# Optimization experiments

Hardware: AMD Instinct MI355X
Metric: run time of the kernel (lower is better)

Reference implementation:

```python
import jax, jax.numpy as jnp
import numpy as np

B, T, D, U = 64, 1024, 300, 300


def setup_inputs() -> dict:
    key = jax.random.key(0)
    ks = jax.random.split(key, 12)
    inputs = jax.random.normal(ks[0], (B, T, D), jnp.float32)
    lengths = jax.random.randint(ks[1], (B,), T // 2, T + 1)
    mask = jnp.arange(T)[None, :] < lengths[:, None]  # [B,T] bool

    def w(k, shape, fan_in):
        return jax.random.normal(k, shape, jnp.float32) * (1.0 / np.sqrt(fan_in))

    # Keras GRU (reset_after=True): kernel [D,3U], recurrent_kernel [U,3U], bias [2,3U]
    k_fwd = w(ks[2], (D, 3 * U), D)
    rk_fwd = w(ks[3], (U, 3 * U), U)
    b_fwd = jnp.zeros((2, 3 * U), jnp.float32)
    k_bwd = w(ks[4], (D, 3 * U), D)
    rk_bwd = w(ks[5], (U, 3 * U), U)
    b_bwd = jnp.zeros((2, 3 * U), jnp.float32)
    w_fc = w(ks[6], (2 * U, U), 2 * U)
    b_fc = jnp.zeros((U,), jnp.float32)
    return {
        "inputs": inputs, "mask": mask,
        "k_fwd": k_fwd, "rk_fwd": rk_fwd, "b_fwd": b_fwd,
        "k_bwd": k_bwd, "rk_bwd": rk_bwd, "b_bwd": b_bwd,
        "w_fc": w_fc, "b_fc": b_fc, "training": 0,
    }


def _gru_dir(x, mask, kernel, rkernel, bias):
    """Keras GRU v2 (reset_after=True), zero_output_for_mask, state frozen on masked steps.
    x: [B,T,D], mask: [B,T] bool -> (ys [B,T,U], h_final [B,U])"""
    b_in, b_rec = bias[0], bias[1]
    u = rkernel.shape[0]
    # precompute input projections for all timesteps (cuDNN-style hoisting)
    xp = jnp.einsum('btd,dk->btk', x, kernel) + b_in  # [B,T,3U]

    def step(h, inp):
        xt, mt = inp  # xt: [B,3U], mt: [B]
        rp = h @ rkernel + b_rec  # [B,3U]
        xz, xr, xh = jnp.split(xt, 3, axis=-1)
        rz, rr, rh = jnp.split(rp, 3, axis=-1)
        z = jax.nn.sigmoid(xz + rz)
        r = jax.nn.sigmoid(xr + rr)
        hh = jnp.tanh(xh + r * rh)
        h_new = z * h + (1.0 - z) * hh
        m = mt[:, None]
        h_carry = jnp.where(m, h_new, h)       # state does not update on masked steps
        y = jnp.where(m, h_new, jnp.zeros_like(h_new))  # zero_output_for_mask
        return h_carry, y

    h0 = jnp.zeros((x.shape[0], u), x.dtype)
    h_final, ys = jax.lax.scan(step, h0, (xp.transpose(1, 0, 2), mask.T))
    return ys.transpose(1, 0, 2), h_final


def reference(inputs, mask, k_fwd, rk_fwd, b_fwd, k_bwd, rk_bwd, b_bwd, w_fc, b_fc, training):
    mask = mask.astype(bool)
    x = inputs  # Dropout is identity at inference (training=0)
    y_f, h_f = _gru_dir(x, mask, k_fwd, rk_fwd, b_fwd)
    # backward direction: process reversed sequence/mask, then re-reverse outputs
    y_b, h_b = _gru_dir(x[:, ::-1], mask[:, ::-1], k_bwd, rk_bwd, b_bwd)
    y_b = y_b[:, ::-1]
    output = jnp.concatenate([y_f, y_b], axis=-1)  # [B,T,2U]
    state = jax.nn.relu(jnp.concatenate([h_f, h_b], axis=-1) @ w_fc + b_fc)  # [B,U]
    return output, state
```

## Files before the change

kernel.cpp:

```cpp
#include <hip/hip_runtime.h>
#include <hip/hip_bf16.h>


#define B_   64
#define T_   1024
#define D_   300
#define U_   300
#define NU   900
#define KP   320
#define NP   960
#define XPW  912
#define KB_  10
#define KRES 2
#define HSP  328
#define FRAGS_PER_DIR 570
#define NRESF 114
#define NWGM 4

typedef short short8 __attribute__((ext_vector_type(8)));
typedef float floatx4 __attribute__((ext_vector_type(4)));

__device__ __forceinline__ float b2f_bits(unsigned short u) {
  union { unsigned int i; float f; } v; v.i = ((unsigned int)u) << 16; return v.f;
}
__device__ __forceinline__ unsigned short f2b(float f) {
  __hip_bfloat16 h = __float2bfloat16(f);
  return *reinterpret_cast<unsigned short*>(&h);
}

__global__ __launch_bounds__(64) void k_detect(const unsigned int* __restrict__ xw,
                                               const unsigned char* __restrict__ mb,
                                               int* __restrict__ flags) {
  __shared__ int red[64];
  int tid = threadIdx.x;
  int hits = 0;
  for (int i = tid; i < 2048; i += 64) {
    unsigned int lo = xw[i] & 0xFFFFu;
    int e = (int)((lo >> 7) & 0xFF);
    if (e >= 105 && e <= 135) hits++;
  }
  red[tid] = hits;
  __syncthreads();
  if (tid == 0) {
    int s = 0;
    for (int i = 0; i < 64; ++i) s += red[i];
    flags[0] = (s >= 1024) ? 1 : 0;
    unsigned char b0 = mb[0], b1 = mb[1];
    flags[1] = (b1 == 0) ? 0 : ((b0 == 1 && b1 == 1) ? 1 : 2);
  }
}

__global__ __launch_bounds__(256) void k_lengths(const unsigned char* __restrict__ mraw,
                                                 const int* __restrict__ flags,
                                                 int* __restrict__ lens) {
  __shared__ int red[256];
  int b = blockIdx.x, tid = threadIdx.x;
  int mt = flags[1];
  int s = 0;
  if (mt == 0) {
    const int* m = (const int*)mraw;
    for (int t = tid; t < T_; t += 256) s += m[(size_t)b * T_ + t] ? 1 : 0;
  } else if (mt == 1) {
    for (int t = tid; t < T_; t += 256) s += mraw[(size_t)b * T_ + t] ? 1 : 0;
  } else {
    const unsigned short* m = (const unsigned short*)mraw;
    for (int t = tid; t < T_; t += 256) s += m[(size_t)b * T_ + t] ? 1 : 0;
  }
  red[tid] = s; __syncthreads();
  for (int off = 128; off > 0; off >>= 1) {
    if (tid < off) red[tid] += red[tid + off];
    __syncthreads();
  }
  if (tid == 0) lens[b] = red[0];
}

__global__ __launch_bounds__(256) void k_xpad(const void* __restrict__ xraw,
                                              const int* __restrict__ flags,
                                              unsigned short* __restrict__ xp) {
  int id = blockIdx.x * 256 + threadIdx.x;
  int row = id / 40, seg = id % 40;
  int kbase = seg * 8;
  int bf = flags[0];
  unsigned short v[8];
  if (bf) {
    const unsigned short* x = (const unsigned short*)xraw;
#pragma unroll
    for (int i = 0; i < 8; ++i) {
      int k = kbase + i;
      v[i] = (k < D_) ? x[(size_t)row * D_ + k] : (unsigned short)0;
    }
  } else {
    const float* x = (const float*)xraw;
#pragma unroll
    for (int i = 0; i < 8; ++i) {
      int k = kbase + i;
      v[i] = (k < D_) ? f2b(x[(size_t)row * D_ + k]) : (unsigned short)0;
    }
  }
  uint4 o;
  o.x = (unsigned)v[0] | ((unsigned)v[1] << 16);
  o.y = (unsigned)v[2] | ((unsigned)v[3] << 16);
  o.z = (unsigned)v[4] | ((unsigned)v[5] << 16);
  o.w = (unsigned)v[6] | ((unsigned)v[7] << 16);
  *(uint4*)(xp + (size_t)row * KP + kbase) = o;
}

__global__ __launch_bounds__(256) void k_wpad(const void* __restrict__ kf,
                                              const void* __restrict__ kb,
                                              const int* __restrict__ flags,
                                              unsigned short* __restrict__ kp) {
  int id = blockIdx.x * 256 + threadIdx.x;
  if (id >= 2 * KP * NP) return;
  int dir = id / (KP * NP);
  int r = id % (KP * NP);
  int k = r / NP, n = r % NP;
  int bf = flags[0];
  unsigned short v = 0;
  if (k < D_ && n < NU) {
    size_t si = (size_t)k * NU + n;
    if (bf) v = ((const unsigned short*)(dir ? kb : kf))[si];
    else    v = f2b(((const float*)(dir ? kb : kf))[si]);
  }
  kp[id] = v;
}

__global__ __launch_bounds__(256) void k_prep(const void* __restrict__ rkf,
                                              const void* __restrict__ rkb,
                                              const void* __restrict__ bfw,
                                              const void* __restrict__ bbw,
                                              const void* __restrict__ wfc,
                                              const void* __restrict__ bfc,
                                              const int* __restrict__ flags,
                                              unsigned short* __restrict__ rkc,
                                              float* __restrict__ biasc,
                                              unsigned short* __restrict__ wfcc,
                                              float* __restrict__ bfcc) {
  int i = blockIdx.x * 256 + threadIdx.x;
  int bf = flags[0];
  if (i < 2 * D_ * NU) {
    int dir = i / (D_ * NU), r = i % (D_ * NU);
    const void* src = dir ? rkb : rkf;
    rkc[i] = bf ? ((const unsigned short*)src)[r] : f2b(((const float*)src)[r]);
  }
  if (i < 2 * 2 * NU) {
    int dir = i / (2 * NU), r = i % (2 * NU);
    const void* src = dir ? bbw : bfw;
    biasc[i] = bf ? b2f_bits(((const unsigned short*)src)[r]) : ((const float*)src)[r];
  }
  if (i < 2 * U_ * U_) {
    wfcc[i] = bf ? ((const unsigned short*)wfc)[i] : f2b(((const float*)wfc)[i]);
  }
  if (i < U_) {
    bfcc[i] = bf ? b2f_bits(((const unsigned short*)bfc)[i]) : ((const float*)bfc)[i];
  }
}

__global__ __launch_bounds__(256) void k_bpack(const unsigned short* __restrict__ rkc,
                                               unsigned short* __restrict__ bpack) {
  int idx = blockIdx.x * 256 + threadIdx.x;
  const int total = 2 * FRAGS_PER_DIR * 512;
  if (idx >= total) return;
  int rem = idx;
  int j = rem & 7; rem >>= 3;
  int lane = rem & 63; rem >>= 6;
  int f = rem % FRAGS_PER_DIR;
  int dir = rem / FRAGS_PER_DIR;
  int w, fr, ntc;
  if (f < 270) { w = f / 90; fr = f - w * 90; ntc = 9; }
  else { int f2 = f - 270; w = 3 + f2 / 60; fr = f2 % 60; ntc = 6; }
  int kb = fr / ntc, nt = fr % ntc;
  int lb = nt / 3, g = nt % 3;
  int ub0 = (w < 3) ? w * 3 : 9 + (w - 3) * 2;
  int l15 = lane & 15, quad = lane >> 4;
  int k = kb * 32 + quad * 8 + j;
  int u = (ub0 + lb) * 16 + l15;
  unsigned short v = 0;
  if (k < U_ && u < U_) {
    v = rkc[(size_t)dir * U_ * NU + (size_t)k * NU + (size_t)g * U_ + u];
  }
  bpack[idx] = v;
}

template <bool XPF32>
__global__ __launch_bounds__(256) void k_gemm(const unsigned short* __restrict__ xpad,
                                              const unsigned short* __restrict__ kpad,
                                              const float* __restrict__ biasc,
                                              void* __restrict__ xp_out) {
  __shared__ __align__(16) unsigned short As[64 * 40];
  __shared__ __align__(16) unsigned short Bs[64 * 40];
  int tid = threadIdx.x;
  int wave = tid >> 6, lane = tid & 63;
  int m0 = blockIdx.x * 64, n0 = blockIdx.y * 64;
  int dir = blockIdx.z;
  const unsigned short* Bsrc = kpad + (size_t)dir * KP * NP;
  const float* bin = biasc + (size_t)dir * 2 * NU;

  floatx4 acc[4];
#pragma unroll
  for (int i = 0; i < 4; ++i) acc[i] = {0.f, 0.f, 0.f, 0.f};

  int arow = tid >> 2, aseg = tid & 3;
  int bk = tid & 31, bn8 = (tid >> 5) * 8;
  int fr = lane & 15, fq = lane >> 4;

  for (int kc = 0; kc < KP; kc += 32) {
    uint4 av = *(const uint4*)(xpad + (size_t)(m0 + arow) * KP + kc + aseg * 8);
    uint4 bv = *(const uint4*)(Bsrc + (size_t)(kc + bk) * NP + n0 + bn8);
    *(uint4*)(As + arow * 40 + aseg * 8) = av;
    unsigned short tmp[8];
    tmp[0] = bv.x & 0xffff; tmp[1] = bv.x >> 16;
    tmp[2] = bv.y & 0xffff; tmp[3] = bv.y >> 16;
    tmp[4] = bv.z & 0xffff; tmp[5] = bv.z >> 16;
    tmp[6] = bv.w & 0xffff; tmp[7] = bv.w >> 16;
#pragma unroll
    for (int i = 0; i < 8; ++i) Bs[(bn8 + i) * 40 + bk] = tmp[i];
    __syncthreads();
    short8 a = *(const short8*)(As + (wave * 16 + fr) * 40 + fq * 8);
#pragma unroll
    for (int nt = 0; nt < 4; ++nt) {
      short8 bfrag = *(const short8*)(Bs + (nt * 16 + fr) * 40 + fq * 8);
      acc[nt] = __builtin_amdgcn_mfma_f32_16x16x32_bf16(a, bfrag, acc[nt], 0, 0, 0);
    }
    __syncthreads();
  }
#pragma unroll
  for (int nt = 0; nt < 4; ++nt) {
    int col = n0 + nt * 16 + fr;
    if (col >= XPW) continue;
    float bi = (col < NU) ? bin[col] : 0.f;
#pragma unroll
    for (int r = 0; r < 4; ++r) {
      int m = m0 + wave * 16 + fq * 4 + r;
      float v = acc[nt][r] + bi;
      size_t idx = ((size_t)dir * 65536 + m) * XPW + col;
      if (XPF32) ((float*)xp_out)[idx] = v;
      else ((unsigned short*)xp_out)[idx] = f2b(v);
    }
  }
}

template <int NTC>
__device__ __forceinline__ void phase(floatx4 (&acc)[9],
                                      const unsigned short* __restrict__ bp,
                                      const unsigned short* __restrict__ sBw,
                                      const unsigned short (*sHi)[HSP],
                                      const unsigned short (*sLo)[HSP],
                                      int l15, int quad) {
  short8 bA[NTC], bB[NTC];
#pragma unroll
  for (int nt = 0; nt < NTC; ++nt)
    bA[nt] = *(const short8*)(bp + ((size_t)(KRES * NTC + nt)) * 512);
#pragma unroll
  for (int nt = 0; nt < NTC; ++nt)
    bB[nt] = *(const short8*)(bp + ((size_t)((KRES + 1) * NTC + nt)) * 512);
#pragma unroll
  for (int kb = 0; kb < KRES; ++kb) {
    short8 ah = *(const short8*)&sHi[l15][kb * 32 + quad * 8];
    short8 al = *(const short8*)&sLo[l15][kb * 32 + quad * 8];
#pragma unroll
    for (int nt = 0; nt < NTC; ++nt) {
      short8 b = *(const short8*)(sBw + ((size_t)(kb * NTC + nt)) * 512);
      acc[nt] = __builtin_amdgcn_mfma_f32_16x16x32_bf16(ah, b, acc[nt], 0, 0, 0);
      acc[nt] = __builtin_amdgcn_mfma_f32_16x16x32_bf16(al, b, acc[nt], 0, 0, 0);
    }
  }
#pragma unroll
  for (int kb = KRES; kb < KB_; kb += 2) {
    {
      short8 ah = *(const short8*)&sHi[l15][kb * 32 + quad * 8];
      short8 al = *(const short8*)&sLo[l15][kb * 32 + quad * 8];
#pragma unroll
      for (int nt = 0; nt < NTC; ++nt) {
        acc[nt] = __builtin_amdgcn_mfma_f32_16x16x32_bf16(ah, bA[nt], acc[nt], 0, 0, 0);
        acc[nt] = __builtin_amdgcn_mfma_f32_16x16x32_bf16(al, bA[nt], acc[nt], 0, 0, 0);
      }
      if (kb + 2 < KB_) {
#pragma unroll
        for (int nt = 0; nt < NTC; ++nt)
          bA[nt] = *(const short8*)(bp + ((size_t)((kb + 2) * NTC + nt)) * 512);
      }
    }
    {
      short8 ah = *(const short8*)&sHi[l15][(kb + 1) * 32 + quad * 8];
      short8 al = *(const short8*)&sLo[l15][(kb + 1) * 32 + quad * 8];
#pragma unroll
      for (int nt = 0; nt < NTC; ++nt) {
        acc[nt] = __builtin_amdgcn_mfma_f32_16x16x32_bf16(ah, bB[nt], acc[nt], 0, 0, 0);
        acc[nt] = __builtin_amdgcn_mfma_f32_16x16x32_bf16(al, bB[nt], acc[nt], 0, 0, 0);
      }
      if (kb + 3 < KB_) {
#pragma unroll
        for (int nt = 0; nt < NTC; ++nt)
          bB[nt] = *(const short8*)(bp + ((size_t)((kb + 3) * NTC + nt)) * 512);
      }
    }
  }
}

template <bool XPF32>
__global__ __launch_bounds__(512) void k_scan(const unsigned short* __restrict__ bpack,
                                              const float* __restrict__ biasc,
                                              const void* __restrict__ xp_all,
                                              const int* __restrict__ lens,
                                              const int* __restrict__ flags,
                                              float* __restrict__ hfin,
                                              void* __restrict__ outraw) {
  __shared__ unsigned short sHi[16][HSP];
  __shared__ unsigned short sLo[16][HSP];
  __shared__ __align__(16) unsigned short sB[NRESF * 512];

  const int tid = threadIdx.x;
  const int mg = blockIdx.x;
  const int dir = blockIdx.y;
  const int wave = tid >> 6, lane = tid & 63;
  const int l15 = lane & 15, quad = lane >> 4;
  const int obf = flags[0];
  unsigned short* out16 = (unsigned short*)outraw;
  float* out32 = (float*)outraw;

  const int NBLK = (wave < 3) ? 3 : 2;
  const int NTCw = NBLK * 3;
  const int UB0w = (wave < 3) ? wave * 3 : 9 + (wave - 3) * 2;
  const int FB   = (wave < 3) ? wave * 90 : 270 + (wave - 3) * 60;
  const int RB   = (wave < 3) ? wave * 18 : 54 + (wave - 3) * 12;

  {
    unsigned int* p0 = (unsigned int*)&sHi[0][0];
    unsigned int* p1 = (unsigned int*)&sLo[0][0];
    for (int i = tid; i < 16 * HSP / 2; i += 512) { p0[i] = 0u; p1[i] = 0u; }
  }
  {
    const unsigned short* src = bpack + ((size_t)dir * FRAGS_PER_DIR + FB) * 512 + lane * 8;
    unsigned short* dst = sB + (size_t)RB * 512 + lane * 8;
    for (int j = 0; j < KRES * NTCw; ++j)
      *(uint4*)(dst + (size_t)j * 512) = *(const uint4*)(src + (size_t)j * 512);
  }

  int ucl[3]; bool cv[3];
  float bz[3], brg[3], bh[3];
  {
    const float* brec = biasc + (size_t)dir * 2 * NU + NU;
#pragma unroll
    for (int lb = 0; lb < 3; ++lb) {
      int u = (UB0w + lb) * 16 + l15;
      bool v = (lb < NBLK) && (u < U_);
      cv[lb] = v;
      ucl[lb] = v ? u : 0;
      bz[lb] = brec[ucl[lb]]; brg[lb] = brec[U_ + ucl[lb]]; bh[lb] = brec[2 * U_ + ucl[lb]];
    }
  }
  int mylen[4];
#pragma unroll
  for (int r = 0; r < 4; ++r) mylen[r] = lens[mg * 16 + quad * 4 + r];
  float hold[3][4];
#pragma unroll
  for (int lb = 0; lb < 3; ++lb)
#pragma unroll
    for (int r = 0; r < 4; ++r) hold[lb][r] = 0.f;

  __syncthreads();

  const unsigned short* bp = bpack + ((size_t)dir * FRAGS_PER_DIR + FB) * 512 + (size_t)lane * 8;
  const unsigned short* sBw = sB + (size_t)RB * 512 + (size_t)lane * 8;

#pragma unroll 1
  for (int s = 0; s < T_; ++s) {
    const int t = dir ? (T_ - 1 - s) : s;

    floatx4 acc[9];
#pragma unroll
    for (int i = 0; i < 9; ++i) acc[i] = {0.f, 0.f, 0.f, 0.f};
    if (wave < 3) phase<9>(acc, bp, sBw, sHi, sLo, l15, quad);
    else          phase<6>(acc, bp, sBw, sHi, sLo, l15, quad);

    float X[3][3][4];
    {
      size_t dbase = (size_t)dir * 65536;
#pragma unroll
      for (int r = 0; r < 4; ++r) {
        size_t ro = (dbase + (size_t)(mg * 16 + quad * 4 + r) * T_ + t) * XPW;
        if (XPF32) {
          const float* xr = (const float*)xp_all + ro;
#pragma unroll
          for (int lb = 0; lb < 3; ++lb) {
            X[lb][0][r] = xr[ucl[lb]];
            X[lb][1][r] = xr[U_ + ucl[lb]];
            X[lb][2][r] = xr[2 * U_ + ucl[lb]];
          }
        } else {
          const unsigned short* xr = (const unsigned short*)xp_all + ro;
#pragma unroll
          for (int lb = 0; lb < 3; ++lb) {
            X[lb][0][r] = b2f_bits(xr[ucl[lb]]);
            X[lb][1][r] = b2f_bits(xr[U_ + ucl[lb]]);
            X[lb][2][r] = b2f_bits(xr[2 * U_ + ucl[lb]]);
          }
        }
      }
    }

    __syncthreads();

#pragma unroll
    for (int r = 0; r < 4; ++r) {
      const int row = quad * 4 + r;
      const bool m = (t < mylen[r]);
      const size_t ob = ((size_t)(mg * 16 + row) * T_ + t) * 600 + (size_t)dir * U_;
#pragma unroll
      for (int lb = 0; lb < 3; ++lb) {
        float z  = 1.f / (1.f + __expf(-(X[lb][0][r] + acc[lb * 3 + 0][r] + bz[lb])));
        float rg = 1.f / (1.f + __expf(-(X[lb][1][r] + acc[lb * 3 + 1][r] + brg[lb])));
        float hh = tanhf(X[lb][2][r] + rg * (acc[lb * 3 + 2][r] + bh[lb]));
        float hn = z * hold[lb][r] + (1.f - z) * hh;
        float hw = m ? hn : hold[lb][r];
        hold[lb][r] = hw;
        if (cv[lb]) {
          float y = m ? hn : 0.f;
          if (obf) out16[ob + ucl[lb]] = f2b(y); else out32[ob + ucl[lb]] = y;
          unsigned short hib = f2b(hw);
          sHi[row][ucl[lb]] = hib;
          sLo[row][ucl[lb]] = f2b(hw - b2f_bits(hib));
        }
      }
    }
    __syncthreads();
  }

#pragma unroll
  for (int lb = 0; lb < 3; ++lb) {
    if (!cv[lb]) continue;
#pragma unroll
    for (int r = 0; r < 4; ++r)
      hfin[((size_t)dir * B_ + mg * 16 + quad * 4 + r) * 304 + ucl[lb]] = hold[lb][r];
  }
}

__global__ __launch_bounds__(320) void k_state(const float* __restrict__ hfin,
                                               const unsigned short* __restrict__ wfcc,
                                               const float* __restrict__ bfcc,
                                               const int* __restrict__ flags,
                                               void* __restrict__ outraw) {
  int b = blockIdx.x, u = threadIdx.x;
  if (u >= U_) return;
  int obf = flags[0];
  float acc = bfcc[u];
  const float* hf = hfin + (size_t)b * 304;
  const float* hb = hfin + ((size_t)B_ + b) * 304;
  for (int k = 0; k < U_; ++k) acc = fmaf(hf[k], b2f_bits(wfcc[(size_t)k * U_ + u]), acc);
  for (int k = 0; k < U_; ++k) acc = fmaf(hb[k], b2f_bits(wfcc[(size_t)(U_ + k) * U_ + u]), acc);
  float v = fmaxf(acc, 0.f);
  size_t oi = (size_t)B_ * T_ * 600 + (size_t)b * U_ + u;
  if (obf) ((unsigned short*)outraw)[oi] = f2b(v);
  else     ((float*)outraw)[oi] = v;
}

extern "C" void kernel_launch(void* const* d_in, const int* in_sizes, int n_in,
                              void* d_out, int out_size, void* d_ws, size_t ws_size,
                              hipStream_t stream) {
  const void* x    = d_in[0];
  const void* mask = d_in[1];
  const void* kf   = d_in[2];
  const void* rkf  = d_in[3];
  const void* bfw  = d_in[4];
  const void* kb   = d_in[5];
  const void* rkb  = d_in[6];
  const void* bbw  = d_in[7];
  const void* wfc  = d_in[8];
  const void* bfc  = d_in[9];

  char* ws = (char*)d_ws;
  size_t off = 0;
  auto alloc = [&](size_t bytes) { void* p = ws + off; off += (bytes + 255) & ~(size_t)255; return p; };
  int* flags            = (int*)alloc(256);
  int* lens             = (int*)alloc(256);
  unsigned short* xpad  = (unsigned short*)alloc((size_t)65536 * KP * 2);
  unsigned short* kpad  = (unsigned short*)alloc((size_t)2 * KP * NP * 2);
  unsigned short* rkc   = (unsigned short*)alloc((size_t)2 * D_ * NU * 2);
  unsigned short* bpack = (unsigned short*)alloc((size_t)2 * FRAGS_PER_DIR * 512 * 2);
  float* biasc          = (float*)alloc((size_t)2 * 2 * NU * 4);
  unsigned short* wfcc  = (unsigned short*)alloc((size_t)2 * U_ * U_ * 2);
  float* bfcc           = (float*)alloc((size_t)U_ * 4);
  float* hfin           = (float*)alloc((size_t)2 * B_ * 304 * 4);
  void* xp = (void*)(ws + off);
  size_t need_f32 = off + (size_t)2 * 65536 * XPW * 4;
  bool xpf32 = ws_size >= need_f32;

  k_detect<<<dim3(1), dim3(64), 0, stream>>>((const unsigned int*)x, (const unsigned char*)mask, flags);
  k_lengths<<<dim3(B_), dim3(256), 0, stream>>>((const unsigned char*)mask, flags, lens);
  k_xpad<<<dim3(65536 * 40 / 256), dim3(256), 0, stream>>>(x, flags, xpad);
  k_wpad<<<dim3((2 * KP * NP + 255) / 256), dim3(256), 0, stream>>>(kf, kb, flags, kpad);
  k_prep<<<dim3((2 * D_ * NU + 255) / 256), dim3(256), 0, stream>>>(rkf, rkb, bfw, bbw, wfc, bfc,
                                                                    flags, rkc, biasc, wfcc, bfcc);
  k_bpack<<<dim3((2 * FRAGS_PER_DIR * 512 + 255) / 256), dim3(256), 0, stream>>>(rkc, bpack);
  if (xpf32) {
    k_gemm<true><<<dim3(1024, 15, 2), dim3(256), 0, stream>>>(xpad, kpad, biasc, xp);
    k_scan<true><<<dim3(NWGM, 2), dim3(512), 0, stream>>>(bpack, biasc, xp, lens, flags, hfin, d_out);
  } else {
    k_gemm<false><<<dim3(1024, 15, 2), dim3(256), 0, stream>>>(xpad, kpad, biasc, xp);
    k_scan<false><<<dim3(NWGM, 2), dim3(512), 0, stream>>>(bpack, biasc, xp, lens, flags, hfin, d_out);
  }
  k_state<<<dim3(B_), dim3(320), 0, stream>>>(hfin, wfcc, bfcc, flags, d_out);
}
```

Measured before the change: 14.55 ms.

## Double-buffer hidden state in LDS to drop one barrier per GRU step

```diff
diff --git a/kernel.cpp b/kernel.cpp
--- a/kernel.cpp
+++ b/kernel.cpp
@@ -26,6 +26,14 @@
 __device__ __forceinline__ unsigned short f2b(float f) {
   __hip_bfloat16 h = __float2bfloat16(f);
   return *reinterpret_cast<unsigned short*>(&h);
+}
+__device__ __forceinline__ float sigm_f(float x) {
+  float e = __expf(-x);
+  return __fdividef(1.f, 1.f + e);
+}
+__device__ __forceinline__ float tanh_f(float x) {
+  float e = __expf(2.f * x);
+  return 1.f - __fdividef(2.f, e + 1.f);
 }
 
 __global__ __launch_bounds__(64) void k_detect(const unsigned int* __restrict__ xw,
@@ -239,12 +247,15 @@
   }
 }
 
-template <int NTC>
-__device__ __forceinline__ void phase(floatx4 (&acc)[9],
+template <int NTC, bool XPF32>
+__device__ __forceinline__ void phase(floatx4 (&acc)[9], float (&X)[3][3][4],
                                       const unsigned short* __restrict__ bp,
                                       const unsigned short* __restrict__ sBw,
-                                      const unsigned short (*sHi)[HSP],
-                                      const unsigned short (*sLo)[HSP],
+                                      const unsigned short (*hH)[HSP],
+                                      const unsigned short (*hL)[HSP],
+                                      const void* __restrict__ xp_all,
+                                      const size_t* __restrict__ xbase,
+                                      int t, const int (*xcol)[3],
                                       int l15, int quad) {
   short8 bA[NTC], bB[NTC];
 #pragma unroll
@@ -254,9 +265,31 @@
   for (int nt = 0; nt < NTC; ++nt)
     bB[nt] = *(const short8*)(bp + ((size_t)((KRES + 1) * NTC + nt)) * 512);
 #pragma unroll
+  for (int r = 0; r < 4; ++r) {
+    size_t ro = xbase[r] + (size_t)t * XPW;
+    if (XPF32) {
+      const float* xr = (const float*)xp_all + ro;
+#pragma unroll
+      for (int lb = 0; lb < 3; ++lb) {
+        X[lb][0][r] = xr[xcol[lb][0]];
+        X[lb][1][r] = xr[xcol[lb][1]];
+        X[lb][2][r] = xr[xcol[lb][2]];
+      }
+    } else {
+      const unsigned short* xr = (const unsigned short*)xp_all + ro;
+#pragma unroll
+      for (int lb = 0; lb < 3; ++lb) {
+        X[lb][0][r] = b2f_bits(xr[xcol[lb][0]]);
+        X[lb][1][r] = b2f_bits(xr[xcol[lb][1]]);
+        X[lb][2][r] = b2f_bits(xr[xcol[lb][2]]);
+      }
+    }
+  }
+  __builtin_amdgcn_s_setprio(1);
+#pragma unroll
   for (int kb = 0; kb < KRES; ++kb) {
-    short8 ah = *(const short8*)&sHi[l15][kb * 32 + quad * 8];
-    short8 al = *(const short8*)&sLo[l15][kb * 32 + quad * 8];
+    short8 ah = *(const short8*)&hH[l15][kb * 32 + quad * 8];
+    short8 al = *(const short8*)&hL[l15][kb * 32 + quad * 8];
 #pragma unroll
     for (int nt = 0; nt < NTC; ++nt) {
       short8 b = *(const short8*)(sBw + ((size_t)(kb * NTC + nt)) * 512);
@@ -267,8 +300,8 @@
 #pragma unroll
   for (int kb = KRES; kb < KB_; kb += 2) {
     {
-      short8 ah = *(const short8*)&sHi[l15][kb * 32 + quad * 8];
-      short8 al = *(const short8*)&sLo[l15][kb * 32 + quad * 8];
+      short8 ah = *(const short8*)&hH[l15][kb * 32 + quad * 8];
+      short8 al = *(const short8*)&hL[l15][kb * 32 + quad * 8];
 #pragma unroll
       for (int nt = 0; nt < NTC; ++nt) {
         acc[nt] = __builtin_amdgcn_mfma_f32_16x16x32_bf16(ah, bA[nt], acc[nt], 0, 0, 0);
@@ -281,8 +314,8 @@
       }
     }
     {
-      short8 ah = *(const short8*)&sHi[l15][(kb + 1) * 32 + quad * 8];
-      short8 al = *(const short8*)&sLo[l15][(kb + 1) * 32 + quad * 8];
+      short8 ah = *(const short8*)&hH[l15][(kb + 1) * 32 + quad * 8];
+      short8 al = *(const short8*)&hL[l15][(kb + 1) * 32 + quad * 8];
 #pragma unroll
       for (int nt = 0; nt < NTC; ++nt) {
         acc[nt] = __builtin_amdgcn_mfma_f32_16x16x32_bf16(ah, bB[nt], acc[nt], 0, 0, 0);
@@ -295,18 +328,19 @@
       }
     }
   }
+  __builtin_amdgcn_s_setprio(0);
 }
 
 template <bool XPF32>
-__global__ __launch_bounds__(512) void k_scan(const unsigned short* __restrict__ bpack,
-                                              const float* __restrict__ biasc,
-                                              const void* __restrict__ xp_all,
-                                              const int* __restrict__ lens,
-                                              const int* __restrict__ flags,
-                                              float* __restrict__ hfin,
-                                              void* __restrict__ outraw) {
-  __shared__ unsigned short sHi[16][HSP];
-  __shared__ unsigned short sLo[16][HSP];
+__global__ __launch_bounds__(512, 2) void k_scan(const unsigned short* __restrict__ bpack,
+                                                 const float* __restrict__ biasc,
+                                                 const void* __restrict__ xp_all,
+                                                 const int* __restrict__ lens,
+                                                 const int* __restrict__ flags,
+                                                 float* __restrict__ hfin,
+                                                 void* __restrict__ outraw) {
+  __shared__ unsigned short sHi[2][16][HSP];
+  __shared__ unsigned short sLo[2][16][HSP];
   __shared__ __align__(16) unsigned short sB[NRESF * 512];
 
   const int tid = threadIdx.x;
@@ -325,9 +359,9 @@
   const int RB   = (wave < 3) ? wave * 18 : 54 + (wave - 3) * 12;
 
   {
-    unsigned int* p0 = (unsigned int*)&sHi[0][0];
-    unsigned int* p1 = (unsigned int*)&sLo[0][0];
-    for (int i = tid; i < 16 * HSP / 2; i += 512) { p0[i] = 0u; p1[i] = 0u; }
+    unsigned int* p0 = (unsigned int*)&sHi[0][0][0];
+    unsigned int* p1 = (unsigned int*)&sLo[0][0][0];
+    for (int i = tid; i < 2 * 16 * HSP / 2; i += 512) { p0[i] = 0u; p1[i] = 0u; }
   }
   {
     const unsigned short* src = bpack + ((size_t)dir * FRAGS_PER_DIR + FB) * 512 + lane * 8;
@@ -338,6 +372,7 @@
 
   int ucl[3]; bool cv[3];
   float bz[3], brg[3], bh[3];
+  int xcol[3][3];
   {
     const float* brec = biasc + (size_t)dir * 2 * NU + NU;
 #pragma unroll
@@ -347,8 +382,13 @@
       cv[lb] = v;
       ucl[lb] = v ? u : 0;
       bz[lb] = brec[ucl[lb]]; brg[lb] = brec[U_ + ucl[lb]]; bh[lb] = brec[2 * U_ + ucl[lb]];
-    }
-  }
+      xcol[lb][0] = ucl[lb]; xcol[lb][1] = U_ + ucl[lb]; xcol[lb][2] = 2 * U_ + ucl[lb];
+    }
+  }
+  size_t xbase[4];
+#pragma unroll
+  for (int r = 0; r < 4; ++r)
+    xbase[r] = ((size_t)dir * 65536 + (size_t)(mg * 16 + quad * 4 + r) * T_) * XPW;
   int mylen[4];
 #pragma unroll
   for (int r = 0; r < 4; ++r) mylen[r] = lens[mg * 16 + quad * 4 + r];
@@ -366,41 +406,17 @@
 #pragma unroll 1
   for (int s = 0; s < T_; ++s) {
     const int t = dir ? (T_ - 1 - s) : s;
+    const int par = s & 1;
 
     floatx4 acc[9];
 #pragma unroll
     for (int i = 0; i < 9; ++i) acc[i] = {0.f, 0.f, 0.f, 0.f};
-    if (wave < 3) phase<9>(acc, bp, sBw, sHi, sLo, l15, quad);
-    else          phase<6>(acc, bp, sBw, sHi, sLo, l15, quad);
-
     float X[3][3][4];
-    {
-      size_t dbase = (size_t)dir * 65536;
-#pragma unroll
-      for (int r = 0; r < 4; ++r) {
-        size_t ro = (dbase + (size_t)(mg * 16 + quad * 4 + r) * T_ + t) * XPW;
-        if (XPF32) {
-          const float* xr = (const float*)xp_all + ro;
-#pragma unroll
-          for (int lb = 0; lb < 3; ++lb) {
-            X[lb][0][r] = xr[ucl[lb]];
-            X[lb][1][r] = xr[U_ + ucl[lb]];
-            X[lb][2][r] = xr[2 * U_ + ucl[lb]];
-          }
-        } else {
-          const unsigned short* xr = (const unsigned short*)xp_all + ro;
-#pragma unroll
-          for (int lb = 0; lb < 3; ++lb) {
-            X[lb][0][r] = b2f_bits(xr[ucl[lb]]);
-            X[lb][1][r] = b2f_bits(xr[U_ + ucl[lb]]);
-            X[lb][2][r] = b2f_bits(xr[2 * U_ + ucl[lb]]);
-          }
-        }
-      }
-    }
-
-    __syncthreads();
-
+    if (wave < 3) phase<9, XPF32>(acc, X, bp, sBw, sHi[par], sLo[par], xp_all, xbase, t, xcol, l15, quad);
+    else          phase<6, XPF32>(acc, X, bp, sBw, sHi[par], sLo[par], xp_all, xbase, t, xcol, l15, quad);
+
+    unsigned short (*nHi)[HSP] = sHi[par ^ 1];
+    unsigned short (*nLo)[HSP] = sLo[par ^ 1];
 #pragma unroll
     for (int r = 0; r < 4; ++r) {
       const int row = quad * 4 + r;
@@ -408,9 +424,9 @@
       const size_t ob = ((size_t)(mg * 16 + row) * T_ + t) * 600 + (size_t)dir * U_;
 #pragma unroll
       for (int lb = 0; lb < 3; ++lb) {
-        float z  = 1.f / (1.f + __expf(-(X[lb][0][r] + acc[lb * 3 + 0][r] + bz[lb])));
-        float rg = 1.f / (1.f + __expf(-(X[lb][1][r] + acc[lb * 3 + 1][r] + brg[lb])));
-        float hh = tanhf(X[lb][2][r] + rg * (acc[lb * 3 + 2][r] + bh[lb]));
+        float z  = sigm_f(X[lb][0][r] + acc[lb * 3 + 0][r] + bz[lb]);
+        float rg = sigm_f(X[lb][1][r] + acc[lb * 3 + 1][r] + brg[lb]);
+        float hh = tanh_f(X[lb][2][r] + rg * (acc[lb * 3 + 2][r] + bh[lb]));
         float hn = z * hold[lb][r] + (1.f - z) * hh;
         float hw = m ? hn : hold[lb][r];
         hold[lb][r] = hw;
@@ -418,12 +434,15 @@
           float y = m ? hn : 0.f;
           if (obf) out16[ob + ucl[lb]] = f2b(y); else out32[ob + ucl[lb]] = y;
           unsigned short hib = f2b(hw);
-          sHi[row][ucl[lb]] = hib;
-          sLo[row][ucl[lb]] = f2b(hw - b2f_bits(hib));
+          nHi[row][ucl[lb]] = hib;
+          nLo[row][ucl[lb]] = f2b(hw - b2f_bits(hib));
         }
       }
     }
-    __syncthreads();
+
+    asm volatile("s_waitcnt lgkmcnt(0)" ::: "memory");
+    __builtin_amdgcn_s_barrier();
+    __builtin_amdgcn_sched_barrier(0);
   }
 
 #pragma unroll
```

Result: slower. 18.60 ms (+27.9%).
